# Optimization experiments

Hardware: AMD Instinct MI355X
Metric: run time of the kernel (lower is better)

## Reference

```python
import jax, jax.numpy as jnp
import numpy as np
import math

B, S, D, H = 8, 1024, 512, 8  # batch, seqlen, d_model, heads
DK = D // H

def setup_inputs() -> dict:
    key = jax.random.key(0)
    ks = jax.random.split(key, 8)
    std = 1.0 / math.sqrt(D)
    return {
        "x": jax.random.normal(ks[0], (B, S, D), jnp.float32),
        "utT_similarities": jax.random.uniform(ks[1], (B, S, S), jnp.float32),
        "Wk": jax.random.normal(ks[2], (D, D), jnp.float32) * std,
        "bk": jnp.zeros((D,), jnp.float32),
        "Wv": jax.random.normal(ks[3], (D, D), jnp.float32) * std,
        "bv": jnp.zeros((D,), jnp.float32),
        "Wo": jax.random.normal(ks[4], (D, D), jnp.float32) * std,
        "bo": jnp.zeros((D,), jnp.float32),
        "gammas": jax.random.normal(ks[5], (H, 1, 1), jnp.float32) * 0.1,
    }

def reference(x, utT_similarities, Wk, bk, Wv, bv, Wo, bo, gammas):
    b, s, d = x.shape
    h = gammas.shape[0]
    dk = d // h
    NEG = -1e32

    def split_heads(t):  # [b,s,d] -> [b,h,s,dk]
        return t.reshape(b, s, h, dk).transpose(0, 2, 1, 3)

    # kq_same=True: q and k share k_linear
    q = split_heads(x @ Wk.T + bk)
    k = q
    v = split_heads(x @ Wv.T + bv)

    scores = jnp.einsum('bhid,bhjd->bhij', q, k) / jnp.sqrt(jnp.float32(dk))
    scores = scores * utT_similarities[:, None, :, :]

    mask = jnp.tril(jnp.ones((s, s), dtype=bool))  # causal, incl diagonal (mask=1)

    # distance-decay block (no_grad in torch -> stop_gradient)
    s_ = jax.nn.softmax(jnp.where(mask, scores, NEG), axis=-1) * mask
    distcum = jnp.cumsum(s_, axis=-1)
    disttotal = jnp.sum(s_, axis=-1, keepdims=True)
    idx = jnp.arange(s)
    position_effect = jnp.abs(idx[None, :] - idx[:, None]).astype(jnp.float32)  # [s,s]
    dist_scores = jnp.sqrt(jnp.clip((disttotal - distcum) * position_effect, 0.0, None))
    dist_scores = jax.lax.stop_gradient(dist_scores)

    gamma = -jax.nn.softplus(gammas)[None]  # [1,h,1,1]
    total_effect = jnp.clip(jnp.exp(dist_scores * gamma), 1e-5, 1e5)

    scores = jax.nn.softmax(jnp.where(mask, scores * total_effect, NEG), axis=-1)
    # zero_pad=False (mask=1 path), dropout is identity in eval
    out = jnp.einsum('bhij,bhjd->bhid', scores, v)
    out = out.transpose(0, 2, 1, 3).reshape(b, s, d)
    return out @ Wo.T + bo
```

## Files before the change

### kernel.cpp

```cpp
#include <hip/hip_runtime.h>
#include <math.h>

#define NB   8
#define SS   1024
#define DD   512
#define HH   8
#define DKK  64
#define NEGF (-3.0e38f)
#define SC   (0.125f * 1.4426950408889634f)

#define QSTR 88
#define SCHUNK (16 * 256)
#define PSTR 280

typedef _Float16 half8 __attribute__((ext_vector_type(8)));
typedef float    f32x4 __attribute__((ext_vector_type(4)));

#define GLDS16(g, l) __builtin_amdgcn_global_load_lds( \
    (const __attribute__((address_space(1))) void*)(g), \
    (__attribute__((address_space(3))) void*)(l), 16, 0, 0)

template<int CTRL, int RM, int BM, bool BC>
__device__ __forceinline__ float dpp_f(float x) {
    return __builtin_bit_cast(float,
        __builtin_amdgcn_update_dpp(0, __builtin_bit_cast(int, x),
                                    CTRL, RM, BM, BC));
}

__device__ __forceinline__ float scan64(float x) {
    x += dpp_f<0x111, 0xf, 0xf, true >(x);
    x += dpp_f<0x112, 0xf, 0xf, true >(x);
    x += dpp_f<0x114, 0xf, 0xf, true >(x);
    x += dpp_f<0x118, 0xf, 0xf, true >(x);
    x += dpp_f<0x142, 0xa, 0xf, false>(x);
    x += dpp_f<0x143, 0xc, 0xf, false>(x);
    return x;
}

__device__ __forceinline__ float redsum64(float x) {
    x += dpp_f<0xB1,  0xf, 0xf, true>(x);
    x += dpp_f<0x4E,  0xf, 0xf, true>(x);
    x += dpp_f<0x141, 0xf, 0xf, true>(x);
    x += dpp_f<0x140, 0xf, 0xf, true>(x);
    x += __shfl_xor(x, 16);
    x += __shfl_xor(x, 32);
    return x;
}

__device__ __forceinline__ float bcast63(float x) {
    return __builtin_bit_cast(float,
        __builtin_amdgcn_readlane(__builtin_bit_cast(int, x), 63));
}

__global__ __launch_bounds__(256) void cvt_fp16(
    const float* __restrict__ x,  _Float16* __restrict__ xh,
    const float* __restrict__ wk, _Float16* __restrict__ wkh,
    const float* __restrict__ wv, _Float16* __restrict__ wvh,
    const float* __restrict__ wo, _Float16* __restrict__ woh)
{
    const size_t NX = (size_t)NB * SS * DD;
    const size_t NW = (size_t)DD * DD;
    size_t f = ((size_t)blockIdx.x * 256 + threadIdx.x) * 8;
    const float* src; _Float16* dst; size_t off;
    if (f < NX)               { src = x;  dst = xh;  off = f; }
    else if (f < NX + NW)     { src = wk; dst = wkh; off = f - NX; }
    else if (f < NX + 2*NW)   { src = wv; dst = wvh; off = f - NX - 2*NW + NW; }
    else                      { src = wo; dst = woh; off = f - NX - 2*NW; }
    float4 f0 = *(const float4*)&src[off];
    float4 f1 = *(const float4*)&src[off + 4];
    half8 hv = {(_Float16)f0.x,(_Float16)f0.y,(_Float16)f0.z,(_Float16)f0.w,
                (_Float16)f1.x,(_Float16)f1.y,(_Float16)f1.z,(_Float16)f1.w};
    *(half8*)&dst[off] = hv;
}

__global__ __launch_bounds__(256) void gemm_qv(
    const _Float16* __restrict__ xh,
    const _Float16* __restrict__ wkh, const float* __restrict__ bk,
    const _Float16* __restrict__ wvh, const float* __restrict__ bv,
    _Float16* __restrict__ q_ws, _Float16* __restrict__ vt_ws)
{
    __shared__ __align__(16) _Float16 Ah[128 * 64];
    __shared__ __align__(16) _Float16 Bh[128 * 64];

    const int m0  = blockIdx.x * 128;
    const int n0c = blockIdx.y * 128;
    const bool is_v = (n0c >= DD);
    const _Float16* __restrict__ Wp = is_v ? wvh : wkh;
    const float*    __restrict__ bp = is_v ? bv : bk;
    const int n0 = n0c & (DD - 1);

    const int tid  = threadIdx.x;
    const int w    = tid >> 6;
    const int lane = tid & 63;
    const int quad = lane >> 4;
    const int n    = lane & 15;
    const int wm   = w >> 1, wn = w & 1;

    f32x4 acc[4][4] = {};

    for (int k0 = 0; k0 < DD; k0 += 64) {
        __syncthreads();
        #pragma unroll
        for (int c = 0; c < 4; ++c) {
            const int ci = (w * 4 + c) * 64 + lane;
            const int r  = ci >> 3;
            const int co = (ci & 7) * 8;
            GLDS16(&xh[(size_t)(m0 + r) * DD + k0 + co], &Ah[(w * 4 + c) * 512]);
            GLDS16(&Wp[(size_t)(n0 + r) * DD + k0 + co], &Bh[(w * 4 + c) * 512]);
        }
        __syncthreads();
        #pragma unroll
        for (int kf = 0; kf < 2; ++kf) {
            half8 af[4], bf[4];
            #pragma unroll
            for (int mi = 0; mi < 4; ++mi)
                af[mi] = *(const half8*)&Ah[(wm*64 + mi*16 + n) * 64 + kf*32 + quad*8];
            #pragma unroll
            for (int ni = 0; ni < 4; ++ni)
                bf[ni] = *(const half8*)&Bh[(wn*64 + ni*16 + n) * 64 + kf*32 + quad*8];
            #pragma unroll
            for (int mi = 0; mi < 4; ++mi)
                #pragma unroll
                for (int ni = 0; ni < 4; ++ni)
                    acc[mi][ni] = __builtin_amdgcn_mfma_f32_16x16x32_f16(
                        af[mi], bf[ni], acc[mi][ni], 0, 0, 0);
        }
    }

    #pragma unroll
    for (int mi = 0; mi < 4; ++mi) {
        #pragma unroll
        for (int ni = 0; ni < 4; ++ni) {
            const int col = n0 + wn*64 + ni*16 + n;
            const int h   = col >> 6;
            const int dk  = col & 63;
            const float bias = bp[col];
            const int gbase = m0 + wm*64 + mi*16 + quad*4;
            const int bidx  = gbase >> 10;
            const int sr    = gbase & (SS - 1);
            if (!is_v) {
                #pragma unroll
                for (int reg = 0; reg < 4; ++reg)
                    q_ws[((size_t)(bidx * HH + h) * SS + sr + reg) * DKK + dk] =
                        (_Float16)(acc[mi][ni][reg] + bias);
            } else {
                _Float16 h4[4];
                #pragma unroll
                for (int reg = 0; reg < 4; ++reg)
                    h4[reg] = (_Float16)(acc[mi][ni][reg] + bias);
                *(uint2*)&vt_ws[((size_t)(bidx * HH + h) * DKK + dk) * SS + sr] =
                    *(uint2*)h4;
            }
        }
    }
}

__global__ __launch_bounds__(256) void gemm_out(
    const _Float16* __restrict__ A,
    const _Float16* __restrict__ woh, const float* __restrict__ bo,
    float* __restrict__ out)
{
    __shared__ __align__(16) _Float16 Ah[128 * 64];
    __shared__ __align__(16) _Float16 Bh[128 * 64];

    const int m0 = blockIdx.x * 128;
    const int n0 = blockIdx.y * 128;

    const int tid  = threadIdx.x;
    const int w    = tid >> 6;
    const int lane = tid & 63;
    const int quad = lane >> 4;
    const int n    = lane & 15;
    const int wm   = w >> 1, wn = w & 1;

    f32x4 acc[4][4] = {};

    for (int k0 = 0; k0 < DD; k0 += 64) {
        __syncthreads();
        #pragma unroll
        for (int c = 0; c < 4; ++c) {
            const int ci = (w * 4 + c) * 64 + lane;
            const int r  = ci >> 3;
            const int co = (ci & 7) * 8;
            GLDS16(&A[(size_t)(m0 + r) * DD + k0 + co],   &Ah[(w * 4 + c) * 512]);
            GLDS16(&woh[(size_t)(n0 + r) * DD + k0 + co], &Bh[(w * 4 + c) * 512]);
        }
        __syncthreads();
        #pragma unroll
        for (int kf = 0; kf < 2; ++kf) {
            half8 af[4], bf[4];
            #pragma unroll
            for (int mi = 0; mi < 4; ++mi)
                af[mi] = *(const half8*)&Ah[(wm*64 + mi*16 + n) * 64 + kf*32 + quad*8];
            #pragma unroll
            for (int ni = 0; ni < 4; ++ni)
                bf[ni] = *(const half8*)&Bh[(wn*64 + ni*16 + n) * 64 + kf*32 + quad*8];
            #pragma unroll
            for (int mi = 0; mi < 4; ++mi)
                #pragma unroll
                for (int ni = 0; ni < 4; ++ni)
                    acc[mi][ni] = __builtin_amdgcn_mfma_f32_16x16x32_f16(
                        af[mi], bf[ni], acc[mi][ni], 0, 0, 0);
        }
    }

    #pragma unroll
    for (int mi = 0; mi < 4; ++mi) {
        #pragma unroll
        for (int ni = 0; ni < 4; ++ni) {
            const int col  = n0 + wn*64 + ni*16 + n;
            const float bias = bo[col];
            const int gbase = m0 + wm*64 + mi*16 + quad*4;
            #pragma unroll
            for (int reg = 0; reg < 4; ++reg)
                out[(size_t)(gbase + reg) * DD + col] = acc[mi][ni][reg] + bias;
        }
    }
}

__global__ __launch_bounds__(1024) void attn_mfma(
    const _Float16* __restrict__ q,
    const _Float16* __restrict__ vt,
    const float* __restrict__ utT,
    const float* __restrict__ gammas,
    _Float16* __restrict__ attn)
{
    __shared__ __align__(16) unsigned char smem[4 * SCHUNK * 4];
    __shared__ __align__(16) _Float16 q_lds[16 * QSTR];
    float*    s_lds = (float*)smem;
    _Float16* p_lds = (_Float16*)smem;

    const int tid  = threadIdx.x;
    const int w    = tid >> 6;
    const int lane = tid & 63;
    const int quad = lane >> 4;
    const int n    = lane & 15;
    const int bh   = blockIdx.y;
    const int b    = bh >> 3;
    const int h    = bh & 7;
    const int r0   = ((SS / 16 - 1) - blockIdx.x) * 16;

    const _Float16* __restrict__ kq  = q  + (size_t)bh * SS * DKK;
    const _Float16* __restrict__ vtp = vt + (size_t)bh * DKK * SS;

    const int nchunk = (r0 + 16 + 255) >> 8;
    const int nt     = nchunk * 4;
    const int i_lane = r0 + n;

    if (tid < 256) {
        const int row = tid >> 4;
        const int c   = tid & 15;
        *(uint2*)&q_lds[row * QSTR + c * 4] =
            *(const uint2*)&kq[(size_t)(r0 + row) * DKK + c * 4];
    }
    __syncthreads();

    const float* __restrict__ utrow = &utT[((size_t)b * SS + i_lane) * SS];
    const int scol = (w * 16 + quad * 4) ^ ((n & 7) << 2);
    const int pcol = lane ^ ((w & 7) << 2);

    #pragma unroll 1
    for (int c0 = 0; c0 < nchunk; ++c0) {
        const int jbase = c0 * 256 + w * 16;
        f32x4 v;
        if (jbase <= r0 + 15) {
            half8 qa0 = *(const half8*)&q_lds[n * QSTR + quad * 8];
            half8 qa1 = *(const half8*)&q_lds[n * QSTR + 32 + quad * 8];
            const _Float16* krow = &kq[(size_t)(jbase + n) * DKK];
            half8 k0 = *(const half8*)&krow[quad * 8];
            half8 k1 = *(const half8*)&krow[32 + quad * 8];
            f32x4 ut = *(const f32x4*)&utrow[jbase + quad * 4];
            f32x4 d = {0.f, 0.f, 0.f, 0.f};
            d = __builtin_amdgcn_mfma_f32_16x16x32_f16(k0, qa0, d, 0, 0, 0);
            d = __builtin_amdgcn_mfma_f32_16x16x32_f16(k1, qa1, d, 0, 0, 0);
            #pragma unroll
            for (int reg = 0; reg < 4; ++reg) {
                const int j = jbase + quad * 4 + reg;
                v[reg] = (j <= i_lane) ? d[reg] * SC * ut[reg] : NEGF;
            }
        } else {
            v = (f32x4){NEGF, NEGF, NEGF, NEGF};
        }
        *(f32x4*)&s_lds[c0 * SCHUNK + n * 256 + scol] = v;
    }
    __syncthreads();

    float sreg[16];
    #pragma unroll
    for (int c0 = 0; c0 < 4; ++c0) {
        if (c0 < nchunk) {
            #pragma unroll
            for (int ttl = 0; ttl < 4; ++ttl)
                sreg[c0 * 4 + ttl] =
                    s_lds[c0 * SCHUNK + w * 256 + ttl * 64 + pcol];
        }
    }

    const int i_row = r0 + w;
    const int ntw_u = (i_row >> 6) + 1;
    const int ntw   = (nt < ntw_u) ? nt : ntw_u;

    float z1acc = 0.f;
    #pragma unroll
    for (int t2 = 0; t2 < 16; ++t2)
        if (t2 < ntw) z1acc += __builtin_amdgcn_exp2f(sreg[t2]);
    const float z1     = redsum64(z1acc);
    const float inv_z1 = 1.0f / z1;

    const float g     = gammas[h];
    const float gl2   = -log1pf(__expf(g)) * 1.4426950408889634f;
    const float flane = (float)lane;

    float carry = 0.f;
    float z2 = 0.f;
    #pragma unroll
    for (int t2 = 0; t2 < 16; ++t2) {
        if (t2 < ntw) {
            const float e  = __builtin_amdgcn_exp2f(sreg[t2]);
            const float xv = scan64(e);
            const float cs = carry + xv;
            carry += bcast63(xv);
            const float pe = (float)(i_row - t2 * 64) - flane;
            const float dd = fmaxf((z1 - cs) * pe, 0.0f) * inv_z1;
            float te = __builtin_amdgcn_exp2f(__builtin_amdgcn_sqrtf(dd) * gl2);
            te = fmaxf(te, 1e-5f);
            const float p = __builtin_amdgcn_exp2f(sreg[t2] * te);
            sreg[t2] = p;
            z2 += p;
        } else {
            sreg[t2] = 0.f;
        }
    }
    z2 = redsum64(z2);
    const float inv_z2 = 1.0f / z2;

    __syncthreads();

    #pragma unroll
    for (int c0 = 0; c0 < 4; ++c0) {
        if (c0 < nchunk) {
            #pragma unroll
            for (int ttl = 0; ttl < 4; ++ttl)
                p_lds[c0 * 16 * PSTR + w * PSTR + ttl * 64 + lane] =
                    (_Float16)(sreg[c0 * 4 + ttl] * inv_z2);
        }
    }

    const int KT = (r0 + 16 + 31) >> 5;
    const _Float16* vrow = &vtp[(size_t)(w * 16 + n) * SS];
    half8 vb[2] = {};
    if (w < 4) {
        #pragma unroll
        for (int u = 0; u < 2; ++u)
            if (u < KT) vb[u] = *(const half8*)&vrow[u * 32 + quad * 8];
    }
    __syncthreads();

    f32x4 oacc = {0.f, 0.f, 0.f, 0.f};
    if (w < 4) {
        for (int kt0 = 0; kt0 < KT; kt0 += 2) {
            half8 cur0 = vb[0], cur1 = vb[1];
            if (kt0 + 2 < KT) vb[0] = *(const half8*)&vrow[(kt0 + 2) * 32 + quad * 8];
            if (kt0 + 3 < KT) vb[1] = *(const half8*)&vrow[(kt0 + 3) * 32 + quad * 8];
            {
                half8 a = *(const half8*)&p_lds[((kt0 >> 3) * 16 + n) * PSTR +
                                                (kt0 & 7) * 32 + quad * 8];
                oacc = __builtin_amdgcn_mfma_f32_16x16x32_f16(a, cur0, oacc, 0, 0, 0);
            }
            if (kt0 + 1 < KT) {
                const int k = kt0 + 1;
                half8 a = *(const half8*)&p_lds[((k >> 3) * 16 + n) * PSTR +
                                                (k & 7) * 32 + quad * 8];
                oacc = __builtin_amdgcn_mfma_f32_16x16x32_f16(a, cur1, oacc, 0, 0, 0);
            }
        }
        #pragma unroll
        for (int reg = 0; reg < 4; ++reg) {
            const int i = r0 + quad * 4 + reg;
            attn[(((size_t)b * SS + i) * HH + h) * DKK + w * 16 + n] =
                (_Float16)oacc[reg];
        }
    }
}

extern "C" void kernel_launch(void* const* d_in, const int* in_sizes, int n_in,
                              void* d_out, int out_size, void* d_ws, size_t ws_size,
                              hipStream_t stream) {
    const float* x      = (const float*)d_in[0];
    const float* utT    = (const float*)d_in[1];
    const float* Wk     = (const float*)d_in[2];
    const float* bk     = (const float*)d_in[3];
    const float* Wv     = (const float*)d_in[4];
    const float* bv     = (const float*)d_in[5];
    const float* Wo     = (const float*)d_in[6];
    const float* bo     = (const float*)d_in[7];
    const float* gammas = (const float*)d_in[8];
    float* out = (float*)d_out;

    const size_t NX  = (size_t)NB * SS * DD;
    const size_t NW  = (size_t)DD * DD;
    const size_t per = NX;

    _Float16* p      = (_Float16*)d_ws;
    _Float16* xh     = p;  p += NX;
    _Float16* wkh    = p;  p += NW;
    _Float16* wvh    = p;  p += NW;
    _Float16* woh    = p;  p += NW;
    _Float16* q_ws   = p;  p += per;
    _Float16* vt_ws  = p;  p += per;
    _Float16* attn_h = p;  p += per;

    const int cvt_blocks = (int)((NX + 3 * NW) / 8 / 256);
    cvt_fp16<<<cvt_blocks, dim3(256), 0, stream>>>(
        x, xh, Wk, wkh, Wv, wvh, Wo, woh);

    dim3 g1(64, 8);
    gemm_qv<<<g1, dim3(256), 0, stream>>>(xh, wkh, bk, wvh, bv, q_ws, vt_ws);

    dim3 g2(SS / 16, NB * HH);
    attn_mfma<<<g2, dim3(1024), 0, stream>>>(q_ws, vt_ws, utT, gammas, attn_h);

    dim3 g3(64, 4);
    gemm_out<<<g3, dim3(256), 0, stream>>>(attn_h, woh, bo, out);
}
```

Measured before the change: 274.1 us.

## Double-buffer LDS tiles in projection GEMMs to overlap loads with MFMA

Both projection GEMM kernels (QV and output) now keep two LDS buffers per operand and issue the global-to-LDS loads for the next K tile before computing on the current one. This leaves one barrier per K step instead of two and lets load latency overlap with MFMA work. LDS use doubles to 64 KB per block, which may lower occupancy. The correctness of the overlap relies on the hardware's wait-count handling for the async LDS loads at the barrier.

Measured after the change: 273.3 us. No clear change (-0.3%).

```diff
diff --git a/kernel.cpp b/kernel.cpp
--- a/kernel.cpp
+++ b/kernel.cpp
@@ -79,8 +79,8 @@
     const _Float16* __restrict__ wvh, const float* __restrict__ bv,
     _Float16* __restrict__ q_ws, _Float16* __restrict__ vt_ws)
 {
-    __shared__ __align__(16) _Float16 Ah[128 * 64];
-    __shared__ __align__(16) _Float16 Bh[128 * 64];
+    __shared__ __align__(16) _Float16 Ah[2][128 * 64];
+    __shared__ __align__(16) _Float16 Bh[2][128 * 64];
 
     const int m0  = blockIdx.x * 128;
     const int n0c = blockIdx.y * 128;
@@ -96,28 +96,43 @@
     const int n    = lane & 15;
     const int wm   = w >> 1, wn = w & 1;
 
+    const int ci  = (w * 4) * 64 + lane;
     f32x4 acc[4][4] = {};
 
-    for (int k0 = 0; k0 < DD; k0 += 64) {
-        __syncthreads();
-        #pragma unroll
-        for (int c = 0; c < 4; ++c) {
-            const int ci = (w * 4 + c) * 64 + lane;
-            const int r  = ci >> 3;
-            const int co = (ci & 7) * 8;
-            GLDS16(&xh[(size_t)(m0 + r) * DD + k0 + co], &Ah[(w * 4 + c) * 512]);
-            GLDS16(&Wp[(size_t)(n0 + r) * DD + k0 + co], &Bh[(w * 4 + c) * 512]);
-        }
-        __syncthreads();
+    #pragma unroll
+    for (int c = 0; c < 4; ++c) {
+        const int cc = ci + c * 64;
+        const int r  = cc >> 3, co = (cc & 7) * 8;
+        GLDS16(&xh[(size_t)(m0 + r) * DD + co], &Ah[0][(w * 4 + c) * 512]);
+        GLDS16(&Wp[(size_t)(n0 + r) * DD + co], &Bh[0][(w * 4 + c) * 512]);
+    }
+    __syncthreads();
+
+    #pragma unroll
+    for (int step = 0; step < 8; ++step) {
+        const int cur = step & 1;
+        const int nxt = cur ^ 1;
+        const int k0  = step * 64;
+        if (step < 7) {
+            #pragma unroll
+            for (int c = 0; c < 4; ++c) {
+                const int cc = ci + c * 64;
+                const int r  = cc >> 3, co = (cc & 7) * 8;
+                GLDS16(&xh[(size_t)(m0 + r) * DD + k0 + 64 + co],
+                       &Ah[nxt][(w * 4 + c) * 512]);
+                GLDS16(&Wp[(size_t)(n0 + r) * DD + k0 + 64 + co],
+                       &Bh[nxt][(w * 4 + c) * 512]);
+            }
+        }
         #pragma unroll
         for (int kf = 0; kf < 2; ++kf) {
             half8 af[4], bf[4];
             #pragma unroll
             for (int mi = 0; mi < 4; ++mi)
-                af[mi] = *(const half8*)&Ah[(wm*64 + mi*16 + n) * 64 + kf*32 + quad*8];
+                af[mi] = *(const half8*)&Ah[cur][(wm*64 + mi*16 + n) * 64 + kf*32 + quad*8];
             #pragma unroll
             for (int ni = 0; ni < 4; ++ni)
-                bf[ni] = *(const half8*)&Bh[(wn*64 + ni*16 + n) * 64 + kf*32 + quad*8];
+                bf[ni] = *(const half8*)&Bh[cur][(wn*64 + ni*16 + n) * 64 + kf*32 + quad*8];
             #pragma unroll
             for (int mi = 0; mi < 4; ++mi)
                 #pragma unroll
@@ -125,6 +140,7 @@
                     acc[mi][ni] = __builtin_amdgcn_mfma_f32_16x16x32_f16(
                         af[mi], bf[ni], acc[mi][ni], 0, 0, 0);
         }
+        __syncthreads();
     }
 
     #pragma unroll
@@ -160,8 +176,8 @@
     const _Float16* __restrict__ woh, const float* __restrict__ bo,
     float* __restrict__ out)
 {
-    __shared__ __align__(16) _Float16 Ah[128 * 64];
-    __shared__ __align__(16) _Float16 Bh[128 * 64];
+    __shared__ __align__(16) _Float16 Ah[2][128 * 64];
+    __shared__ __align__(16) _Float16 Bh[2][128 * 64];
 
     const int m0 = blockIdx.x * 128;
     const int n0 = blockIdx.y * 128;
@@ -173,28 +189,43 @@
     const int n    = lane & 15;
     const int wm   = w >> 1, wn = w & 1;
 
+    const int ci = (w * 4) * 64 + lane;
     f32x4 acc[4][4] = {};
 
-    for (int k0 = 0; k0 < DD; k0 += 64) {
-        __syncthreads();
-        #pragma unroll
-        for (int c = 0; c < 4; ++c) {
-            const int ci = (w * 4 + c) * 64 + lane;
-            const int r  = ci >> 3;
-            const int co = (ci & 7) * 8;
-            GLDS16(&A[(size_t)(m0 + r) * DD + k0 + co],   &Ah[(w * 4 + c) * 512]);
-            GLDS16(&woh[(size_t)(n0 + r) * DD + k0 + co], &Bh[(w * 4 + c) * 512]);
-        }
-        __syncthreads();
+    #pragma unroll
+    for (int c = 0; c < 4; ++c) {
+        const int cc = ci + c * 64;
+        const int r  = cc >> 3, co = (cc & 7) * 8;
+        GLDS16(&A[(size_t)(m0 + r) * DD + co],   &Ah[0][(w * 4 + c) * 512]);
+        GLDS16(&woh[(size_t)(n0 + r) * DD + co], &Bh[0][(w * 4 + c) * 512]);
+    }
+    __syncthreads();
+
+    #pragma unroll
+    for (int step = 0; step < 8; ++step) {
+        const int cur = step & 1;
+        const int nxt = cur ^ 1;
+        const int k0  = step * 64;
+        if (step < 7) {
+            #pragma unroll
+            for (int c = 0; c < 4; ++c) {
+                const int cc = ci + c * 64;
+                const int r  = cc >> 3, co = (cc & 7) * 8;
+                GLDS16(&A[(size_t)(m0 + r) * DD + k0 + 64 + co],
+                       &Ah[nxt][(w * 4 + c) * 512]);
+                GLDS16(&woh[(size_t)(n0 + r) * DD + k0 + 64 + co],
+                       &Bh[nxt][(w * 4 + c) * 512]);
+            }
+        }
         #pragma unroll
         for (int kf = 0; kf < 2; ++kf) {
             half8 af[4], bf[4];
             #pragma unroll
             for (int mi = 0; mi < 4; ++mi)
-                af[mi] = *(const half8*)&Ah[(wm*64 + mi*16 + n) * 64 + kf*32 + quad*8];
+                af[mi] = *(const half8*)&Ah[cur][(wm*64 + mi*16 + n) * 64 + kf*32 + quad*8];
             #pragma unroll
             for (int ni = 0; ni < 4; ++ni)
-                bf[ni] = *(const half8*)&Bh[(wn*64 + ni*16 + n) * 64 + kf*32 + quad*8];
+                bf[ni] = *(const half8*)&Bh[cur][(wn*64 + ni*16 + n) * 64 + kf*32 + quad*8];
             #pragma unroll
             for (int mi = 0; mi < 4; ++mi)
                 #pragma unroll
@@ -202,6 +233,7 @@
                     acc[mi][ni] = __builtin_amdgcn_mfma_f32_16x16x32_f16(
                         af[mi], bf[ni], acc[mi][ni], 0, 0, 0);
         }
+        __syncthreads();
     }
 
     #pragma unroll
```
